# Kernel tuning notes

Hardware: AMD Instinct MI355X
Metric: run time of the kernel (lower is better)

## Reference

```python
import jax, jax.numpy as jnp
import numpy as np

B, C, T, W, H = 2, 256, 16, 64, 64


def setup_inputs():
    key = jax.random.key(0)
    ks = jax.random.split(key, 6)
    C2 = C // 2
    return {
        "x": jax.random.normal(ks[0], (B, C, T, W, H), jnp.float32),
        "Wq": jax.random.normal(ks[1], (3, C2, C), jnp.float32) * 0.02,
        "bq": jnp.zeros((3, C2), jnp.float32),
        "Wk": jax.random.normal(ks[2], (3, C2, C), jnp.float32) * 0.02,
        "bk": jnp.zeros((3, C2), jnp.float32),
        "Wv": jax.random.normal(ks[3], (3, C, C), jnp.float32) * 0.02,
        "bv": jnp.zeros((3, C), jnp.float32),
        "gamma": jax.random.normal(ks[4], (3,), jnp.float32) * 0.1,
    }


def _conv1x1(t, Wm, b):
    # Conv3d with kernel_size=1 == per-voxel channel matmul
    return jnp.einsum('bcijk,oc->boijk', t, Wm) + b[None, :, None, None, None]


def _pool(t):
    # MaxPool3d(kernel=(2,1,1), stride=(2,1,1)) along dim 2 (even length)
    return jnp.maximum(t[:, :, 0::2], t[:, :, 1::2])


def _cell(x, Wq, bq, Wk, bk, Wv, bv, gamma, attn_id):
    Bb, Cc, Tt, Ww, Hh = x.shape
    if attn_id == 'T':
        out = x
    elif attn_id == 'W':
        out = jnp.swapaxes(x, 2, 3)  # [B,C,W,T,H]
    else:
        out = jnp.swapaxes(x, 2, 4)  # [B,C,H,W,T]
    A = out.shape[2]
    # NOTE: these are raw row-major reshapes, faithful to torch .view
    q = _conv1x1(out, Wq, bq).reshape(Bb, A, -1)              # [B, A, C/2*d1*d2]
    k = _pool(_conv1x1(out, Wk, bk)).reshape(Bb, -1, A // 2)  # [B, C/2*d1*d2, A/2]
    attn = jax.nn.softmax(jnp.einsum('bij,bjk->bik', q, k), axis=-1)  # [B, A, A/2]
    v = _pool(_conv1x1(out, Wv, bv)).reshape(Bb, -1, A // 2)  # [B, C*d1*d2, A/2]
    o = jnp.einsum('bxp,bap->bxa', v, attn)                   # [B, X, A]
    if attn_id == 'T':
        o = o.reshape(Bb, Cc, Ww, Hh, Tt).transpose(0, 1, 4, 2, 3)
    elif attn_id == 'W':
        o = o.reshape(Bb, Cc, Tt, Hh, Ww).transpose(0, 1, 2, 4, 3)
    else:
        o = o.reshape(Bb, Cc, Tt, Ww, Hh)
    return gamma * o + x


def reference(x, Wq, bq, Wk, bk, Wv, bv, gamma):
    out = x
    for i, aid in enumerate(('T', 'W', 'H')):
        out = _cell(out, Wq[i], bq[i], Wk[i], bk[i], Wv[i], bv[i], gamma[i], aid)
    return out
```

## Files before the change

kernel.cpp:

```cpp
#include <hip/hip_runtime.h>


constexpr int XBS = 16777216;

typedef __attribute__((ext_vector_type(8)))  short short8v;
typedef __attribute__((ext_vector_type(16))) float f32x16;

__device__ __forceinline__ unsigned rne16(float f) {
    unsigned u = __float_as_uint(f);
    return (u + 0x7FFFu + ((u >> 16) & 1u)) >> 16;
}

__global__ __launch_bounds__(64) void prep_w(
    const float* __restrict__ W, unsigned int* __restrict__ dst)
{
    const int l = threadIdx.x;
    const int ks = blockIdx.x, mf = blockIdx.y, hl = blockIdx.z;
    const float* src = W + (mf * 32 + (l & 31)) * 256 + ks * 16 + ((l >> 5) << 3);
    unsigned pk[4];
    #pragma unroll
    for (int e = 0; e < 4; ++e) {
        float f0 = src[2 * e], f1 = src[2 * e + 1];
        unsigned b0, b1;
        if (hl == 0) {
            b0 = __float_as_uint(f0) >> 16;
            b1 = __float_as_uint(f1) >> 16;
        } else {
            unsigned h0 = __float_as_uint(f0) & 0xFFFF0000u;
            unsigned h1 = __float_as_uint(f1) & 0xFFFF0000u;
            b0 = rne16(f0 - __uint_as_float(h0));
            b1 = rne16(f1 - __uint_as_float(h1));
        }
        pk[e] = b0 | (b1 << 16);
    }
    size_t off = ((size_t)(mf * 16 + ks) * 2 + hl) * 256 + l * 4;
    *(uint4*)&dst[off] = make_uint4(pk[0], pk[1], pk[2], pk[3]);
}

template<int CELL>
__global__ __launch_bounds__(256) void xsplit_kernel(
    const float* __restrict__ src, unsigned int* __restrict__ xTp)
{
    __shared__ float T[64][66];
    const int tid = threadIdx.x;
    const int b = blockIdx.z, cb = blockIdx.y, nb = blockIdx.x;
    const int runbase = (CELL == 0) ? nb * 64
                                    : ((nb & 15) * 4096 + ((nb >> 4) << 6));
    const float* sp = src + (size_t)b * XBS + (size_t)(cb * 64) * 65536 + runbase;
    #pragma unroll
    for (int i = 0; i < 4; ++i) {
        int id = tid + i * 256;
        int cl = id >> 4, rc = (id & 15) * 4;
        const float4 v = *(const float4*)&sp[(size_t)cl * 65536 + rc];
        *(float2*)&T[cl][rc]     = make_float2(v.x, v.y);
        *(float2*)&T[cl][rc + 2] = make_float2(v.z, v.w);
    }
    __syncthreads();
    unsigned int* dst = xTp + (size_t)b * (65536u * 256u);
    #pragma unroll
    for (int ps = 0; ps < 4; ++ps) {
        int r = ps * 16 + (tid >> 4);
        int c0 = (tid & 15) * 4;
        unsigned pk[4];
        #pragma unroll
        for (int e = 0; e < 4; ++e) {
            float f = T[c0 + e][r];
            unsigned hi = __float_as_uint(f) & 0xFFFF0000u;
            pk[e] = hi | rne16(f - __uint_as_float(hi));
        }
        int n_row = (CELL == 2) ? (r * 1024 + nb) : (nb * 64 + r);
        *(uint4*)&dst[(size_t)n_row * 256 + cb * 64 + c0] =
            make_uint4(pk[0], pk[1], pk[2], pk[3]);
    }
}

template<bool POOL, int LGS>
__global__ __launch_bounds__(256, 2) void mconv(
    const unsigned int* __restrict__ xTp, const unsigned int* __restrict__ wf,
    const float* __restrict__ bias, float* __restrict__ out, int obs)
{
    constexpr int NS = POOL ? 32768 : 65536;
    constexpr int MF = POOL ? 2 : 4;
    constexpr int NV = POOL ? 2 : 1;

    __shared__ __align__(16) unsigned short Bh[128 * 64];
    __shared__ __align__(16) unsigned short Bl[128 * 64];

    const int tid = threadIdx.x;
    const int lane = tid & 63, wv = tid >> 6;
    const int b = blockIdx.z, gy = blockIdx.y, nb = blockIdx.x;
    const unsigned int* xb = xTp + (size_t)b * (65536u * 256u);

    f32x16 acc[MF][NV];
    #pragma unroll
    for (int m = 0; m < MF; ++m)
        #pragma unroll
        for (int v = 0; v < NV; ++v)
            #pragma unroll
            for (int r = 0; r < 16; ++r) acc[m][v][r] = 0.f;

    for (int ko = 0; ko < 4; ++ko) {
        const int c0u = ko * 64;
        #pragma unroll
        for (int i = 0; i < 8; ++i) {
            int id = tid + i * 256;
            int row = id >> 4, q4 = id & 15;
            int n_src;
            if (!POOL) n_src = nb * 128 + row;
            else {
                int v = row >> 6, m = nb * 64 + (row & 63);
                int p = m >> LGS, s = m & ((1 << LGS) - 1);
                n_src = ((2 * p + v) << LGS) + s;
            }
            const uint4 g = *(const uint4*)&xb[(size_t)n_src * 256 + c0u + q4 * 4];
            unsigned h01 = (g.x >> 16)     | (g.y & 0xFFFF0000u);
            unsigned h23 = (g.z >> 16)     | (g.w & 0xFFFF0000u);
            unsigned l01 = (g.x & 0xFFFFu) | (g.y << 16);
            unsigned l23 = (g.z & 0xFFFFu) | (g.w << 16);
            int byt = row * 128 + (((q4 >> 1) ^ (row & 7)) << 4) + ((q4 & 1) << 3);
            *(uint2*)((char*)Bh + byt) = make_uint2(h01, h23);
            *(uint2*)((char*)Bl + byt) = make_uint2(l01, l23);
        }
        __syncthreads();
        #pragma unroll
        for (int ks = 0; ks < 4; ++ks) {
            short8v ah[MF], al[MF];
            #pragma unroll
            for (int m = 0; m < MF; ++m) {
                int mfG = gy * 4 + (POOL ? ((wv >> 1) * 2 + m) : m);
                const unsigned int* ap =
                    wf + (size_t)((mfG * 16 + ko * 4 + ks) * 2) * 256 + lane * 4;
                ah[m] = *(const short8v*)ap;
                al[m] = *(const short8v*)(ap + 256);
            }
            #pragma unroll
            for (int v = 0; v < NV; ++v) {
                int row = POOL ? (v * 64 + (wv & 1) * 32 + (lane & 31))
                               : (wv * 32 + (lane & 31));
                int byt = row * 128 + (((ks * 2 + (lane >> 5)) ^ (row & 7)) << 4);
                short8v bh = *(const short8v*)((char*)Bh + byt);
                short8v bl = *(const short8v*)((char*)Bl + byt);
                #pragma unroll
                for (int m = 0; m < MF; ++m) {
                    acc[m][v] = __builtin_amdgcn_mfma_f32_32x32x16_bf16(ah[m], bh, acc[m][v], 0, 0, 0);
                    acc[m][v] = __builtin_amdgcn_mfma_f32_32x32x16_bf16(ah[m], bl, acc[m][v], 0, 0, 0);
                    acc[m][v] = __builtin_amdgcn_mfma_f32_32x32x16_bf16(al[m], bh, acc[m][v], 0, 0, 0);
                }
            }
        }
        __syncthreads();
    }

    float* ob = out + (size_t)b * obs;
    const int colbase = POOL ? (nb * 64 + (wv & 1) * 32 + (lane & 31))
                             : (nb * 128 + wv * 32 + (lane & 31));
    #pragma unroll
    for (int m = 0; m < MF; ++m) {
        int mfG = gy * 4 + (POOL ? ((wv >> 1) * 2 + m) : m);
        #pragma unroll
        for (int r = 0; r < 16; ++r) {
            int o = mfG * 32 + (r & 3) + 8 * (r >> 2) + 4 * (lane >> 5);
            float val = POOL ? fmaxf(acc[m][0][r], acc[m][1][r]) : acc[m][0][r];
            ob[(size_t)o * NS + colbase] = val + bias[o];
        }
    }
}

template<int A, int AH, int PP, int G, int KS, int M>
__global__ __launch_bounds__(256) void logits_kernel(
    const float* __restrict__ qb, const float* __restrict__ kb,
    float* __restrict__ Lpart)
{
    const int tid = threadIdx.x;
    const int jl = tid & 63, pg = tid >> 6;
    const int p0 = pg * PP;
    const int b = blockIdx.z, a0 = blockIdx.y * G, kc = blockIdx.x;
    constexpr int CH = M / KS;
    const float* q = qb + (size_t)b * 8388608 + (size_t)a0 * M + (size_t)kc * CH;
    const float* k = kb + (size_t)b * 4194304;

    float acc[G][PP];
    #pragma unroll
    for (int g = 0; g < G; ++g)
        #pragma unroll
        for (int pp = 0; pp < PP; ++pp) acc[g][pp] = 0.f;

    for (int it = 0; it < CH / 64; ++it) {
        const int jo = jl + it * 64;
        const int j  = kc * CH + jo;
        float qv[G];
        #pragma unroll
        for (int g = 0; g < G; ++g) qv[g] = q[g * M + jo];
        float kv[PP];
        if (PP == 8) {
            float4 k0 = *(const float4*)&k[(size_t)j * AH + p0];
            float4 k1 = *(const float4*)&k[(size_t)j * AH + p0 + 4];
            kv[0]=k0.x; kv[1]=k0.y; kv[2]=k0.z; kv[3]=k0.w;
            kv[4]=k1.x; kv[5]=k1.y; kv[6]=k1.z; kv[7]=k1.w;
        } else {
            float2 k0 = *(const float2*)&k[(size_t)j * AH + p0];
            kv[0]=k0.x; if (PP > 1) kv[1]=k0.y;
        }
        #pragma unroll
        for (int g = 0; g < G; ++g)
            #pragma unroll
            for (int pp = 0; pp < PP; ++pp) acc[g][pp] += qv[g] * kv[pp];
    }

    #pragma unroll
    for (int g = 0; g < G; ++g)
        #pragma unroll
        for (int pp = 0; pp < PP; ++pp) {
            float v = acc[g][pp];
            #pragma unroll
            for (int off = 32; off; off >>= 1) v += __shfl_down(v, off, 64);
            if (jl == 0)
                Lpart[(size_t)(((b * A + a0 + g) * AH) + p0 + pp) * KS + kc] = v;
        }
}

__global__ __launch_bounds__(64) void softmax_kernel(
    const float* __restrict__ Lpart, float* __restrict__ attn,
    int AH, int KS)
{
    const int row = blockIdx.x;
    const int p = threadIdx.x;
    float s = 0.f;
    if (p < AH) {
        const size_t base = (size_t)(row * AH + p) * KS;
        for (int kc = 0; kc < KS; ++kc) s += Lpart[base + kc];
    }
    float m = (p < AH) ? s : -3.4e38f;
    #pragma unroll
    for (int off = 32; off; off >>= 1) m = fmaxf(m, __shfl_xor(m, off, 64));
    float e = (p < AH) ? __expf(s - m) : 0.f;
    float t = e;
    #pragma unroll
    for (int off = 32; off; off >>= 1) t += __shfl_xor(t, off, 64);
    if (p < AH) attn[(size_t)row * AH + p] = e / t;
}

template<int CELL>
__global__ __launch_bounds__(256) void apply_kernel(
    const float* __restrict__ vbuf, const float* __restrict__ attn,
    const float* __restrict__ xsrc, float* __restrict__ xdst,
    const float* __restrict__ gp, int gidx)
{
    constexpr int A  = (CELL == 0) ? 16 : 64;
    constexpr int AH = A / 2;
    constexpr int d1 = (CELL == 0) ? 64 : (CELL == 1) ? 16 : 64;
    constexpr int d2 = (CELL == 0) ? 64 : (CELL == 1) ? 64 : 16;
    constexpr int IT = (CELL == 1) ? 4 : 8;

    __shared__ float attnT[AH * (A + 1)];
    __shared__ float vls[d2 * (AH + 1)];

    const int tid = threadIdx.x;
    const int b = blockIdx.z, c = blockIdx.y;
    const int i0 = blockIdx.x * IT;

    for (int idx = tid; idx < A * AH; idx += 256) {
        int a = idx / AH, p = idx % AH;
        attnT[p * (A + 1) + a] = attn[(size_t)b * A * AH + idx];
    }

    const float g = gp[gidx];

    for (int it = 0; it < IT; ++it) {
        const int i = i0 + it;
        __syncthreads();
        const size_t vst = (size_t)b * 8388608 + (size_t)((c * d1 + i) * d2) * AH;
        for (int idx = tid; idx < d2 * AH; idx += 256)
            vls[(idx / AH) * (AH + 1) + (idx % AH)] = vbuf[vst + idx];
        __syncthreads();

        if (CELL < 2) {
            const int jj = tid & 63, wg = tid >> 6;
            float vr[AH];
            #pragma unroll
            for (int p = 0; p < AH; ++p) vr[p] = vls[jj * (AH + 1) + p];
            #pragma unroll
            for (int r = 0; r < A / 4; ++r) {
                int a = wg + r * 4;
                float acc = 0.f;
                #pragma unroll
                for (int p = 0; p < AH; ++p) acc += vr[p] * attnT[p * (A + 1) + a];
                size_t xi = (size_t)b * XBS + c * 65536 +
                            ((CELL == 0) ? a * 4096 + i * 64 : i * 4096 + a * 64) + jj;
                xdst[xi] = g * acc + xsrc[xi];
            }
        } else {
            const int al = tid & 63, jg = tid >> 6;
            float ar[AH];
            #pragma unroll
            for (int p = 0; p < AH; ++p) ar[p] = attnT[p * (A + 1) + al];
            #pragma unroll
            for (int r = 0; r < 4; ++r) {
                int j = jg + r * 4;
                float acc = 0.f;
                #pragma unroll
                for (int p = 0; p < AH; ++p) acc += vls[j * (AH + 1) + p] * ar[p];
                size_t xi = (size_t)b * XBS + c * 65536 + i * 1024 + j * 64 + al;
                xdst[xi] = g * acc + xsrc[xi];
            }
        }
    }
}

extern "C" void kernel_launch(void* const* d_in, const int* in_sizes, int n_in,
                              void* d_out, int out_size, void* d_ws, size_t ws_size,
                              hipStream_t stream)
{
    const float* x  = (const float*)d_in[0];
    const float* Wq = (const float*)d_in[1];
    const float* bq = (const float*)d_in[2];
    const float* Wk = (const float*)d_in[3];
    const float* bk = (const float*)d_in[4];
    const float* Wv = (const float*)d_in[5];
    const float* bv = (const float*)d_in[6];
    const float* gm = (const float*)d_in[7];
    float* out = (float*)d_out;

    float* ws   = (float*)d_ws;
    float* qbuf = ws;
    float* kbuf = qbuf + 16777216;
    float* vbuf = kbuf + 8388608;
    float* Lp   = vbuf + 16777216;
    float* attn = Lp + 65536;
    unsigned int* wfb = (unsigned int*)(attn + 4096);
    unsigned int* xTp = wfb + 3 * 131072;

    dim3 B256(256), B64(64);

    for (int c = 0; c < 3; ++c) {
        unsigned int* wfc = wfb + c * 131072;
        prep_w<<<dim3(16,4,2),B64,0,stream>>>(Wq + c*32768, wfc);
        prep_w<<<dim3(16,4,2),B64,0,stream>>>(Wk + c*32768, wfc + 32768);
        prep_w<<<dim3(16,8,2),B64,0,stream>>>(Wv + c*65536, wfc + 65536);
    }

    xsplit_kernel<0><<<dim3(1024,4,2),B256,0,stream>>>(x, xTp);
    mconv<false,12><<<dim3(512,1,2),B256,0,stream>>>(xTp, wfb,          bq, qbuf, 8388608);
    mconv<true ,12><<<dim3(512,1,2),B256,0,stream>>>(xTp, wfb + 32768,  bk, kbuf, 4194304);
    mconv<true ,12><<<dim3(512,2,2),B256,0,stream>>>(xTp, wfb + 65536,  bv, vbuf, 8388608);
    logits_kernel<16,8,2,8,64,524288><<<dim3(64,2,2),B256,0,stream>>>(qbuf, kbuf, Lp);
    softmax_kernel<<<dim3(32),B64,0,stream>>>(Lp, attn, 8, 64);
    apply_kernel<0><<<dim3(8,256,2),B256,0,stream>>>(vbuf, attn, x, out, gm, 0);

    unsigned int* wf1 = wfb + 131072;
    xsplit_kernel<1><<<dim3(1024,4,2),B256,0,stream>>>(out, xTp);
    mconv<false,10><<<dim3(512,1,2),B256,0,stream>>>(xTp, wf1,          bq+128, qbuf, 8388608);
    mconv<true ,10><<<dim3(512,1,2),B256,0,stream>>>(xTp, wf1 + 32768,  bk+128, kbuf, 4194304);
    mconv<true ,10><<<dim3(512,2,2),B256,0,stream>>>(xTp, wf1 + 65536,  bv+256, vbuf, 8388608);
    logits_kernel<64,32,8,8,16,131072><<<dim3(16,8,2),B256,0,stream>>>(qbuf, kbuf, Lp);
    softmax_kernel<<<dim3(128),B64,0,stream>>>(Lp, attn, 32, 16);
    apply_kernel<1><<<dim3(4,256,2),B256,0,stream>>>(vbuf, attn, out, out, gm, 1);

    unsigned int* wf2 = wfb + 262144;
    xsplit_kernel<2><<<dim3(1024,4,2),B256,0,stream>>>(out, xTp);
    mconv<false,10><<<dim3(512,1,2),B256,0,stream>>>(xTp, wf2,          bq+256, qbuf, 8388608);
    mconv<true ,10><<<dim3(512,1,2),B256,0,stream>>>(xTp, wf2 + 32768,  bk+256, kbuf, 4194304);
    mconv<true ,10><<<dim3(512,2,2),B256,0,stream>>>(xTp, wf2 + 65536,  bv+512, vbuf, 8388608);
    logits_kernel<64,32,8,8,16,131072><<<dim3(16,8,2),B256,0,stream>>>(qbuf, kbuf, Lp);
    softmax_kernel<<<dim3(128),B64,0,stream>>>(Lp, attn, 32, 16);
    apply_kernel<2><<<dim3(8,256,2),B256,0,stream>>>(vbuf, attn, out, out, gm, 2);
}
```

Measured before the change: 1.349 ms.

## Register-tile apply kernel with 4x4 outputs, float4 IO, and swizzled LDS

Rewrites the attention-apply kernel so each thread computes a 4x4 tile of outputs (rows by attention positions) held in registers. V and attention rows are loaded with float4 from global memory or shared memory, and the residual read and output write are also float4. Cell 0 reads V straight from global memory with no LDS staging. Cells 1 and 2 stage V in LDS with an XOR swizzle to avoid bank conflicts. The goal is to cut LDS traffic and scalar memory instructions, at the cost of higher register pressure and a changed per-block work split.

Result: faster. 1.268 ms (-6.1%).

```diff
diff --git a/kernel.cpp b/kernel.cpp
--- a/kernel.cpp
+++ b/kernel.cpp
@@ -248,60 +248,129 @@
 {
     constexpr int A  = (CELL == 0) ? 16 : 64;
     constexpr int AH = A / 2;
-    constexpr int d1 = (CELL == 0) ? 64 : (CELL == 1) ? 16 : 64;
-    constexpr int d2 = (CELL == 0) ? 64 : (CELL == 1) ? 64 : 16;
-    constexpr int IT = (CELL == 1) ? 4 : 8;
-
-    __shared__ float attnT[AH * (A + 1)];
-    __shared__ float vls[d2 * (AH + 1)];
+    constexpr int PADA = AH + 4;
+    constexpr int ITERS = (CELL == 1) ? 4 : 2;
+
+    __shared__ float attnA[A * PADA];
+    __shared__ float vls[(CELL == 0) ? 4 : 64 * 32];
 
     const int tid = threadIdx.x;
     const int b = blockIdx.z, c = blockIdx.y;
-    const int i0 = blockIdx.x * IT;
-
-    for (int idx = tid; idx < A * AH; idx += 256) {
-        int a = idx / AH, p = idx % AH;
-        attnT[p * (A + 1) + a] = attn[(size_t)b * A * AH + idx];
+
+    for (int idx = tid; idx < A * AH / 4; idx += 256) {
+        int a = idx / (AH / 4), q = idx % (AH / 4);
+        *(float4*)&attnA[a * PADA + q * 4] =
+            *(const float4*)&attn[(size_t)b * A * AH + a * AH + q * 4];
     }
 
     const float g = gp[gidx];
-
-    for (int it = 0; it < IT; ++it) {
-        const int i = i0 + it;
+    const float* xs = xsrc + (size_t)b * XBS + (size_t)c * 65536;
+    float*       xd = xdst + (size_t)b * XBS + (size_t)c * 65536;
+    const float* vb = vbuf + (size_t)b * 8388608;
+
+    if (CELL == 0) {
         __syncthreads();
-        const size_t vst = (size_t)b * 8388608 + (size_t)((c * d1 + i) * d2) * AH;
-        for (int idx = tid; idx < d2 * AH; idx += 256)
-            vls[(idx / AH) * (AH + 1) + (idx % AH)] = vbuf[vst + idx];
-        __syncthreads();
-
-        if (CELL < 2) {
-            const int jj = tid & 63, wg = tid >> 6;
-            float vr[AH];
-            #pragma unroll
-            for (int p = 0; p < AH; ++p) vr[p] = vls[jj * (AH + 1) + p];
-            #pragma unroll
-            for (int r = 0; r < A / 4; ++r) {
-                int a = wg + r * 4;
-                float acc = 0.f;
-                #pragma unroll
-                for (int p = 0; p < AH; ++p) acc += vr[p] * attnT[p * (A + 1) + a];
-                size_t xi = (size_t)b * XBS + c * 65536 +
-                            ((CELL == 0) ? a * 4096 + i * 64 : i * 4096 + a * 64) + jj;
-                xdst[xi] = g * acc + xsrc[xi];
-            }
-        } else {
-            const int al = tid & 63, jg = tid >> 6;
-            float ar[AH];
-            #pragma unroll
-            for (int p = 0; p < AH; ++p) ar[p] = attnT[p * (A + 1) + al];
-            #pragma unroll
-            for (int r = 0; r < 4; ++r) {
-                int j = jg + r * 4;
-                float acc = 0.f;
-                #pragma unroll
-                for (int p = 0; p < AH; ++p) acc += vls[j * (AH + 1) + p] * ar[p];
-                size_t xi = (size_t)b * XBS + c * 65536 + i * 1024 + j * 64 + al;
-                xdst[xi] = g * acc + xsrc[xi];
+        const int i0 = blockIdx.x * 8;
+        const int r0 = (tid & 63) * 4;
+        const int il = r0 >> 6, j0 = r0 & 63;
+        const int a0 = (tid >> 6) * 4;
+        float4 aa[2][4];
+        #pragma unroll
+        for (int ch = 0; ch < 2; ++ch)
+            #pragma unroll
+            for (int at = 0; at < 4; ++at)
+                aa[ch][at] = *(const float4*)&attnA[(a0 + at) * PADA + ch * 4];
+        for (int ig = 0; ig < 2; ++ig) {
+            const int i = i0 + ig * 4 + il;
+            const float* vrow = vb + ((size_t)(c * 64 + i) * 64 + j0) * 8;
+            float acc[4][4];
+            #pragma unroll
+            for (int rt = 0; rt < 4; ++rt)
+                #pragma unroll
+                for (int at = 0; at < 4; ++at) acc[rt][at] = 0.f;
+            #pragma unroll
+            for (int ch = 0; ch < 2; ++ch)
+                #pragma unroll
+                for (int rt = 0; rt < 4; ++rt) {
+                    float4 vv = *(const float4*)&vrow[rt * 8 + ch * 4];
+                    #pragma unroll
+                    for (int at = 0; at < 4; ++at)
+                        acc[rt][at] += vv.x * aa[ch][at].x + vv.y * aa[ch][at].y
+                                     + vv.z * aa[ch][at].z + vv.w * aa[ch][at].w;
+                }
+            #pragma unroll
+            for (int at = 0; at < 4; ++at) {
+                int a = a0 + at;
+                size_t xi = (size_t)a * 4096 + i * 64 + j0;
+                float4 sv = *(const float4*)&xs[xi];
+                *(float4*)&xd[xi] = make_float4(
+                    g * acc[0][at] + sv.x, g * acc[1][at] + sv.y,
+                    g * acc[2][at] + sv.z, g * acc[3][at] + sv.w);
+            }
+        }
+    } else {
+        const int k = tid & 15, r0 = k * 4;
+        const int a0 = (tid >> 4) * 4;
+        for (int itn = 0; itn < ITERS; ++itn) {
+            const int ib = (CELL == 1) ? (blockIdx.x * 4 + itn)
+                                       : ((blockIdx.x * 2 + itn) * 4);
+            __syncthreads();
+            {
+                const int rowbase = c * 1024 + ib * ((CELL == 1) ? 64 : 16);
+                const float* src = vb + (size_t)rowbase * 32;
+                int rr = tid >> 3, cc = tid & 7;
+                #pragma unroll
+                for (int u = 0; u < 2; ++u) {
+                    int r = rr + u * 32;
+                    int slot = cc ^ ((r >> 2) & 7);
+                    *(float4*)&vls[r * 32 + slot * 4] =
+                        *(const float4*)&src[r * 32 + cc * 4];
+                }
+            }
+            __syncthreads();
+            float acc[4][4];
+            #pragma unroll
+            for (int rt = 0; rt < 4; ++rt)
+                #pragma unroll
+                for (int at = 0; at < 4; ++at) acc[rt][at] = 0.f;
+            #pragma unroll
+            for (int ch = 0; ch < 8; ++ch) {
+                const int slot = (ch ^ (k & 7)) * 4;
+                float4 aa[4];
+                #pragma unroll
+                for (int at = 0; at < 4; ++at)
+                    aa[at] = *(const float4*)&attnA[(a0 + at) * PADA + ch * 4];
+                #pragma unroll
+                for (int rt = 0; rt < 4; ++rt) {
+                    float4 vv = *(const float4*)&vls[(r0 + rt) * 32 + slot];
+                    #pragma unroll
+                    for (int at = 0; at < 4; ++at)
+                        acc[rt][at] += vv.x * aa[at].x + vv.y * aa[at].y
+                                     + vv.z * aa[at].z + vv.w * aa[at].w;
+                }
+            }
+            if (CELL == 1) {
+                const int i = ib, j0 = r0;
+                #pragma unroll
+                for (int at = 0; at < 4; ++at) {
+                    int a = a0 + at;
+                    size_t xi = (size_t)i * 4096 + a * 64 + j0;
+                    float4 sv = *(const float4*)&xs[xi];
+                    *(float4*)&xd[xi] = make_float4(
+                        g * acc[0][at] + sv.x, g * acc[1][at] + sv.y,
+                        g * acc[2][at] + sv.z, g * acc[3][at] + sv.w);
+                }
+            } else {
+                #pragma unroll
+                for (int rt = 0; rt < 4; ++rt) {
+                    int r = r0 + rt;
+                    int i = ib + (r >> 4), j = r & 15;
+                    size_t xi = (size_t)i * 1024 + j * 64 + a0;
+                    float4 sv = *(const float4*)&xs[xi];
+                    *(float4*)&xd[xi] = make_float4(
+                        g * acc[rt][0] + sv.x, g * acc[rt][1] + sv.y,
+                        g * acc[rt][2] + sv.z, g * acc[rt][3] + sv.w);
+                }
             }
         }
     }
```
